# Kernel optimization log

Measured on AMD Instinct MI355X. Metric: run time of the kernel, lower is better.

The kernel has to match this reference:

```python
import jax, jax.numpy as jnp
import numpy as np

B, C, H, W = 4, 128, 64, 64


def setup_inputs() -> dict:
    key = jax.random.key(0)
    ks = jax.random.split(key, 7)
    s = 1.0 / np.sqrt(C)
    return {
        "x": jax.random.normal(ks[0], (B, C, H, W), dtype=jnp.float32),
        "Wq": jax.random.normal(ks[1], (C, C), dtype=jnp.float32) * s,
        "bq": jnp.zeros((C,), dtype=jnp.float32),
        "Wk": jax.random.normal(ks[2], (C, C), dtype=jnp.float32) * s,
        "bk": jnp.zeros((C,), dtype=jnp.float32),
        "Wv": jax.random.normal(ks[3], (C, C), dtype=jnp.float32) * s,
        "bv": jnp.zeros((C,), dtype=jnp.float32),
    }


def reference(x, Wq, bq, Wk, bk, Wv, bv):
    b, c, h, w = x.shape
    n = h * w
    scale = c ** (-0.5)
    # tokens: [B, N, C]
    xt = x.reshape(b, c, n).transpose(0, 2, 1)
    # 1x1 convs == per-token channel GEMMs (out[c'] = sum_c W[c',c] x[c] + b[c'])
    q = jnp.einsum("bnc,dc->bnd", xt, Wq) + bq  # [B, N, C]
    k = jnp.einsum("bnc,dc->bnd", xt, Wk) + bk  # [B, N, C]
    v = jnp.einsum("bnc,dc->bnd", xt, Wv) + bv  # [B, N, C]
    scores = jnp.einsum("bic,bjc->bij", q, k) * scale  # [B, N, N]
    attn = jax.nn.softmax(scores, axis=-1)
    out = jnp.einsum("bij,bjc->bic", attn, v)  # [B, N, C]
    return out.transpose(0, 2, 1).reshape(b, c, h, w)
```

## Files before the change

kernel.cpp:

```cpp
#include <hip/hip_runtime.h>
#include <hip/hip_bf16.h>


#define BATCH 4
#define CH    128
#define NTOK  4096
#define TK    64
#define SCALE 0.08838834764831845f
#define LOG2E 1.4426950408889634f
#define MFIX  16.0f

typedef __attribute__((ext_vector_type(8)))  short short8;
typedef __attribute__((ext_vector_type(4)))  float f32x4;
typedef __attribute__((ext_vector_type(16))) float f32x16;

static __device__ __forceinline__ unsigned short f2bf(float f) {
    __hip_bfloat16 h = (__hip_bfloat16)f;
    return *(const unsigned short*)&h;
}

static __device__ __forceinline__ unsigned cvt_pk_bf16(float lo, float hi) {
    unsigned r;
    asm("v_cvt_pk_bf16_f32 %0, %1, %2" : "=v"(r) : "v"(lo), "v"(hi));
    return r;
}

static __device__ __forceinline__ short8 pack_bf16x8(float4 a, float4 b) {
    union { unsigned u[4]; short8 s8; } f;
    f.u[0] = cvt_pk_bf16(a.x, a.y);
    f.u[1] = cvt_pk_bf16(a.z, a.w);
    f.u[2] = cvt_pk_bf16(b.x, b.y);
    f.u[3] = cvt_pk_bf16(b.z, b.w);
    return f.s8;
}

__global__ __launch_bounds__(256) void proj_mfma_kernel(
    const float* __restrict__ x,
    const float* __restrict__ Wq, const float* __restrict__ Wk,
    const float* __restrict__ Wv,
    const float* __restrict__ bq, const float* __restrict__ bk,
    const float* __restrict__ bv,
    unsigned short* __restrict__ q_ws, unsigned short* __restrict__ k_ws,
    unsigned short* __restrict__ vt_ws)
{
    __shared__ __align__(16) unsigned short Wl[CH * CH];
    __shared__ __align__(16) unsigned short XsT[64 * CH];

    const int t    = threadIdx.x;
    const int w    = t >> 6;
    const int lane = t & 63;
    const int quad = lane >> 4;
    const int c16  = lane & 15;
    const int n0   = blockIdx.x * 64;
    const int b    = blockIdx.y;
    const int z    = blockIdx.z;
    const float* xb = x + (size_t)b * CH * NTOK;
    const float* wm = (z == 0) ? Wq : (z == 1) ? Wk : Wv;

    #pragma unroll
    for (int i = 0; i < 8; ++i) {
        const int f   = i * 256 + t;
        const int row = f >> 4;
        const int u   = f & 15;
        const float* src = wm + f * 8;
        const float4 a = *(const float4*)src;
        const float4 c = *(const float4*)(src + 4);
        *(short8*)&Wl[row * CH + (u ^ (row & 15)) * 8] = pack_bf16x8(a, c);
    }

    {
        const int tok = lane;
        #pragma unroll
        for (int cc = 0; cc < 4; ++cc) {
            const int cb = 32 * w + 8 * cc;
            float xv[8];
            #pragma unroll
            for (int j = 0; j < 8; ++j)
                xv[j] = xb[(size_t)(cb + j) * NTOK + n0 + tok];
            union { unsigned u[4]; short8 s8; } pk;
            #pragma unroll
            for (int j = 0; j < 4; ++j)
                pk.u[j] = cvt_pk_bf16(xv[2 * j], xv[2 * j + 1]);
            const int phys = ((cb >> 3) ^ (tok & 15));
            *(short8*)&XsT[tok * CH + phys * 8] = pk.s8;
        }
    }
    __syncthreads();

    if (z < 2) {
        const float* bias = (z == 0) ? bq : bk;
        unsigned short* dst = (z == 0) ? q_ws : k_ws;
        const float mul = (z == 0) ? (SCALE * LOG2E) : 1.0f;

        short8 xa[4];
        #pragma unroll
        for (int ks = 0; ks < 4; ++ks)
            xa[ks] = *(const short8*)&XsT[(16 * w + c16) * CH + (((4 * ks + quad) ^ c16) << 3)];

        #pragma unroll
        for (int nt = 0; nt < 8; ++nt) {
            f32x4 a = (f32x4){0.f, 0.f, 0.f, 0.f};
            #pragma unroll
            for (int ks = 0; ks < 4; ++ks) {
                const short8 bf = *(const short8*)
                    &Wl[(16 * nt + c16) * CH + (((4 * ks + quad) ^ c16) << 3)];
                a = __builtin_amdgcn_mfma_f32_16x16x32_bf16(xa[ks], bf, a, 0, 0, 0);
            }
            const float bvv = bias[16 * nt + c16];
            #pragma unroll
            for (int r = 0; r < 4; ++r) {
                const int n = n0 + 16 * w + quad * 4 + r;
                dst[((size_t)b * NTOK + n) * CH + 16 * nt + c16] =
                    f2bf((a[r] + bvv) * mul);
            }
        }
    } else {
        #pragma unroll
        for (int nt = 0; nt < 4; ++nt) {
            short8 xbf[4];
            #pragma unroll
            for (int ks = 0; ks < 4; ++ks)
                xbf[ks] = *(const short8*)&XsT[(16 * nt + c16) * CH + (((4 * ks + quad) ^ c16) << 3)];
            #pragma unroll
            for (int mt = 0; mt < 2; ++mt) {
                const int crow16 = 16 * (2 * w + mt);
                f32x4 acc = (f32x4){0.f, 0.f, 0.f, 0.f};
                #pragma unroll
                for (int ks = 0; ks < 4; ++ks) {
                    const short8 wva = *(const short8*)
                        &Wl[(crow16 + c16) * CH + (((4 * ks + quad) ^ c16) << 3)];
                    acc = __builtin_amdgcn_mfma_f32_16x16x32_bf16(wva, xbf[ks], acc, 0, 0, 0);
                }
                #pragma unroll
                for (int r = 0; r < 4; ++r) {
                    const int crow = crow16 + quad * 4 + r;
                    vt_ws[((size_t)b * CH + crow) * NTOK + n0 + 16 * nt + c16] =
                        f2bf(acc[r] + bv[crow]);
                }
            }
        }
    }
}

template <int SPLIT>
__global__ __launch_bounds__(256, 2) void flash_attn_mfma(
    const unsigned short* __restrict__ q_ws,
    const unsigned short* __restrict__ k_ws,
    const unsigned short* __restrict__ vt_ws,
    float* __restrict__ out,
    float* __restrict__ Op, float* __restrict__ l_p)
{
    __shared__ __align__(16) unsigned short KsU[2][TK * CH];
    __shared__ __align__(16) unsigned short VtU[2][CH * TK];

    const int t    = threadIdx.x;
    const int w    = t >> 6;
    const int lane = t & 63;
    const int half = lane >> 5;
    const int l32  = lane & 31;
    const int jc   = blockIdx.y;
    const int b    = blockIdx.z;
    const int n0   = blockIdx.x * 128;
    const int jbeg = jc * (NTOK / SPLIT);
    constexpr int NT = (NTOK / SPLIT) / TK;

    const unsigned short* kg = k_ws  + (size_t)b * NTOK * CH;
    const unsigned short* vg = vt_ws + (size_t)b * CH * NTOK;

    short8 qa[8];
    {
        const unsigned short* qrow =
            q_ws + ((size_t)b * NTOK + n0 + 32 * w + l32) * CH;
        #pragma unroll
        for (int ks = 0; ks < 8; ++ks)
            qa[ks] = *(const short8*)(qrow + ks * 16 + half * 8);
    }

    f32x16 Oa[4];
    #pragma unroll
    for (int ct = 0; ct < 4; ++ct) Oa[ct] = (f32x16)(0.0f);
    float lsum = 0.f;

    const int krl = lane >> 4, ku = lane & 15;
    const int vcl = lane >> 3, vu = lane & 7;

    auto STAGE = [&](int buf, int jj) {
        #pragma unroll
        for (int ci = 0; ci < 4; ++ci) {
            const int row = 16 * w + 4 * ci + krl;
            const int g   = ku ^ (row & 15);
            const unsigned short* src = kg + (size_t)(jj + row) * CH + g * 8;
            __builtin_amdgcn_global_load_lds(
                (const __attribute__((address_space(1))) void*)src,
                (__attribute__((address_space(3))) void*)&KsU[buf][(16 * w + 4 * ci) * CH],
                16, 0, 0);
        }
        #pragma unroll
        for (int ci = 0; ci < 4; ++ci) {
            const int c = 32 * w + 8 * ci + vcl;
            const int g = vu ^ (c & 7);
            const unsigned short* src = vg + (size_t)c * NTOK + jj + g * 8;
            __builtin_amdgcn_global_load_lds(
                (const __attribute__((address_space(1))) void*)src,
                (__attribute__((address_space(3))) void*)&VtU[buf][(32 * w + 8 * ci) * TK],
                16, 0, 0);
        }
    };

    STAGE(0, jbeg);

    int j0 = jbeg;
    for (int tt = 0; tt < NT; ++tt, j0 += TK) {
        const int cur = tt & 1;
        if (tt + 1 < NT) {
            STAGE(cur ^ 1, j0 + TK);
            asm volatile("s_waitcnt vmcnt(8)" ::: "memory");
        } else {
            asm volatile("s_waitcnt vmcnt(0)" ::: "memory");
        }
        __builtin_amdgcn_sched_barrier(0);
        __builtin_amdgcn_s_barrier();
        __builtin_amdgcn_sched_barrier(0);

        const unsigned short* Kc = &KsU[cur][0];
        const unsigned short* Vc = &VtU[cur][0];

        f32x16 s[2];
        s[0] = (f32x16)(-MFIX);
        s[1] = (f32x16)(-MFIX);
        #pragma unroll
        for (int ks = 0; ks < 8; ++ks) {
            const int ph = (2 * ks + half) ^ (l32 & 15);
            const short8 kf0 = *(const short8*)&Kc[l32 * CH + ph * 8];
            const short8 kf1 = *(const short8*)&Kc[(32 + l32) * CH + ph * 8];
            s[0] = __builtin_amdgcn_mfma_f32_32x32x16_bf16(kf0, qa[ks], s[0], 0, 0, 0);
            s[1] = __builtin_amdgcn_mfma_f32_32x32x16_bf16(kf1, qa[ks], s[1], 0, 0, 0);
        }

        short8 pb[4];
        #pragma unroll
        for (int kt = 0; kt < 2; ++kt) {
            float p[16];
            #pragma unroll
            for (int r = 0; r < 16; ++r) p[r] = exp2f(s[kt][r]);
            float a0 = 0.f, a1 = 0.f, a2 = 0.f, a3 = 0.f;
            #pragma unroll
            for (int r = 0; r < 4; ++r) {
                a0 += p[r]; a1 += p[4 + r]; a2 += p[8 + r]; a3 += p[12 + r];
            }
            lsum += (a0 + a1) + (a2 + a3);
            unsigned wd[8];
            #pragma unroll
            for (int i = 0; i < 8; ++i) wd[i] = cvt_pk_bf16(p[2 * i], p[2 * i + 1]);
            auto r02 = __builtin_amdgcn_permlane32_swap(wd[0], wd[2], false, false);
            auto r13 = __builtin_amdgcn_permlane32_swap(wd[1], wd[3], false, false);
            auto r46 = __builtin_amdgcn_permlane32_swap(wd[4], wd[6], false, false);
            auto r57 = __builtin_amdgcn_permlane32_swap(wd[5], wd[7], false, false);
            union { unsigned u[4]; short8 s8; } f0, f1;
            f0.u[0] = r02[0]; f0.u[1] = r13[0]; f0.u[2] = r02[1]; f0.u[3] = r13[1];
            f1.u[0] = r46[0]; f1.u[1] = r57[0]; f1.u[2] = r46[1]; f1.u[3] = r57[1];
            pb[2 * kt + 0] = f0.s8;
            pb[2 * kt + 1] = f1.s8;
        }

        #pragma unroll
        for (int ks2 = 0; ks2 < 4; ++ks2) {
            #pragma unroll
            for (int ct = 0; ct < 4; ++ct) {
                const int ch = 32 * ct + l32;
                const int ph = (2 * ks2 + half) ^ (ch & 7);
                const short8 vf = *(const short8*)&Vc[ch * TK + ph * 8];
                Oa[ct] = __builtin_amdgcn_mfma_f32_32x32x16_bf16(vf, pb[ks2], Oa[ct], 0, 0, 0);
            }
        }
        __builtin_amdgcn_sched_barrier(0);
        __builtin_amdgcn_s_barrier();
        __builtin_amdgcn_sched_barrier(0);
    }

    const float lt = lsum + __shfl_xor(lsum, 32);
    const int n = n0 + 32 * w + l32;

    if constexpr (SPLIT == 1) {
        const float inv = 1.0f / lt;
        #pragma unroll
        for (int ct = 0; ct < 4; ++ct) {
            #pragma unroll
            for (int r = 0; r < 16; ++r) {
                const int c = 32 * ct + (r & 3) + 8 * (r >> 2) + 4 * half;
                out[((size_t)b * CH + c) * NTOK + n] = Oa[ct][r] * inv;
            }
        }
    } else {
        const size_t chunk = (size_t)(b * SPLIT + jc);
        #pragma unroll
        for (int ct = 0; ct < 4; ++ct) {
            #pragma unroll
            for (int r = 0; r < 16; ++r) {
                const int c = 32 * ct + (r & 3) + 8 * (r >> 2) + 4 * half;
                Op[(chunk * CH + c) * NTOK + n] = Oa[ct][r];
            }
        }
        if (half == 0) l_p[chunk * NTOK + n] = lt;
    }
}

template <int SPLIT>
__global__ __launch_bounds__(256) void combine_kernel(
    const float* __restrict__ Op, const float* __restrict__ l_p,
    float* __restrict__ out)
{
    const int b = blockIdx.y;
    const size_t idx = ((size_t)blockIdx.x * 256 + threadIdx.x) * 4;
    const int c = (int)(idx >> 12);
    const int n = (int)(idx & (NTOK - 1));
    float4 acc = make_float4(0.f, 0.f, 0.f, 0.f);
    float4 den = make_float4(0.f, 0.f, 0.f, 0.f);
    #pragma unroll
    for (int j = 0; j < SPLIT; ++j) {
        const size_t chunk = (size_t)(b * SPLIT + j);
        const float4 o = *(const float4*)&Op[(chunk * CH + c) * NTOK + n];
        const float4 d = *(const float4*)&l_p[chunk * NTOK + n];
        acc.x += o.x; acc.y += o.y; acc.z += o.z; acc.w += o.w;
        den.x += d.x; den.y += d.y; den.z += d.z; den.w += d.w;
    }
    float4 r;
    r.x = acc.x / den.x; r.y = acc.y / den.y;
    r.z = acc.z / den.z; r.w = acc.w / den.w;
    *(float4*)&out[((size_t)b * CH * NTOK) + idx] = r;
}

extern "C" void kernel_launch(void* const* d_in, const int* in_sizes, int n_in,
                              void* d_out, int out_size, void* d_ws, size_t ws_size,
                              hipStream_t stream) {
    const float* x  = (const float*)d_in[0];
    const float* Wq = (const float*)d_in[1];
    const float* bq = (const float*)d_in[2];
    const float* Wk = (const float*)d_in[3];
    const float* bk = (const float*)d_in[4];
    const float* Wv = (const float*)d_in[5];
    const float* bv = (const float*)d_in[6];
    float* out = (float*)d_out;

    const size_t QKV = (size_t)BATCH * NTOK * CH;
    unsigned short* q_ws  = (unsigned short*)d_ws;
    unsigned short* k_ws  = q_ws + QKV;
    unsigned short* vt_ws = k_ws + QKV;
    float* Op = (float*)(vt_ws + QKV);

    const size_t baseBytes = 3 * QKV * 2;
    auto needBytes = [&](size_t S) {
        return baseBytes + S * BATCH * NTOK * (size_t)(CH * 4 + 4);
    };

    dim3 gp(NTOK / 64, BATCH, 3);
    proj_mfma_kernel<<<gp, 256, 0, stream>>>(x, Wq, Wk, Wv, bq, bk, bv,
                                             q_ws, k_ws, vt_ws);

    dim3 gc(CH * NTOK / 1024, BATCH);
    if (ws_size >= needBytes(4)) {
        float* l_p = Op + (size_t)4 * BATCH * NTOK * CH;
        dim3 ga(NTOK / 128, 4, BATCH);
        flash_attn_mfma<4><<<ga, 256, 0, stream>>>(q_ws, k_ws, vt_ws, out, Op, l_p);
        combine_kernel<4><<<gc, 256, 0, stream>>>(Op, l_p, out);
    } else if (ws_size >= needBytes(2)) {
        float* l_p = Op + (size_t)2 * BATCH * NTOK * CH;
        dim3 ga(NTOK / 128, 2, BATCH);
        flash_attn_mfma<2><<<ga, 256, 0, stream>>>(q_ws, k_ws, vt_ws, out, Op, l_p);
        combine_kernel<2><<<gc, 256, 0, stream>>>(Op, l_p, out);
    } else {
        dim3 ga(NTOK / 128, 1, BATCH);
        flash_attn_mfma<1><<<ga, 256, 0, stream>>>(q_ws, k_ws, vt_ws, out,
                                                   nullptr, nullptr);
    }
}
```

Baseline: 126.9 us.

## Fuse projection, split attention and combine into one persistent kernel with grid barriers

Replaces the three-launch sequence (projection, split-K flash attention, combine) with a single persistent 512-block kernel. Two software grid barriers built on atomic counters separate the phases, and the projection and attention phases share LDS through a union. The aim is to remove kernel launch gaps and tail effects between stages. In exchange it adds a memset launch, relies on all 512 blocks being co-resident (two per CU) or the barrier deadlocks, and runs the projection phase unevenly, with some blocks doing two units of work.

```diff
diff --git a/kernel.cpp b/kernel.cpp
--- a/kernel.cpp
+++ b/kernel.cpp
@@ -9,6 +9,7 @@
 #define SCALE 0.08838834764831845f
 #define LOG2E 1.4426950408889634f
 #define MFIX  16.0f
+#define GRID  512
 
 typedef __attribute__((ext_vector_type(8)))  short short8;
 typedef __attribute__((ext_vector_type(4)))  float f32x4;
@@ -32,6 +33,318 @@
     f.u[2] = cvt_pk_bf16(b.x, b.y);
     f.u[3] = cvt_pk_bf16(b.z, b.w);
     return f.s8;
+}
+
+static __device__ __forceinline__ void grid_barrier(unsigned* cnt, unsigned* gen) {
+    __syncthreads();
+    __threadfence();
+    if (threadIdx.x == 0) {
+        unsigned prev = __hip_atomic_fetch_add(cnt, 1u, __ATOMIC_ACQ_REL,
+                                               __HIP_MEMORY_SCOPE_AGENT);
+        if (prev == GRID - 1) {
+            __hip_atomic_store(gen, 1u, __ATOMIC_RELEASE,
+                               __HIP_MEMORY_SCOPE_AGENT);
+        } else {
+            while (__hip_atomic_load(gen, __ATOMIC_ACQUIRE,
+                                     __HIP_MEMORY_SCOPE_AGENT) == 0u) {}
+        }
+    }
+    __syncthreads();
+    __threadfence();
+}
+
+__global__ __launch_bounds__(256, 2) void fused_kernel(
+    const float* __restrict__ x,
+    const float* __restrict__ Wq, const float* __restrict__ Wk,
+    const float* __restrict__ Wv,
+    const float* __restrict__ bq, const float* __restrict__ bk,
+    const float* __restrict__ bv,
+    unsigned short* __restrict__ q_ws, unsigned short* __restrict__ k_ws,
+    unsigned short* __restrict__ vt_ws,
+    float* __restrict__ out, float* __restrict__ Op, float* __restrict__ l_p,
+    unsigned* __restrict__ bar)
+{
+    union SMem {
+        struct { unsigned short Wl[CH * CH]; unsigned short XsT[64 * CH]; } p1;
+        struct { unsigned short K[2][TK * CH]; unsigned short V[2][CH * TK]; } p2;
+    };
+    __shared__ __align__(16) SMem sm;
+
+    const int t   = threadIdx.x;
+    const int bid = blockIdx.x;
+
+    {
+        const int w    = t >> 6;
+        const int lane = t & 63;
+        const int quad = lane >> 4;
+        const int c16  = lane & 15;
+        const int nun  = (bid < 256) ? 2 : 1;
+
+        for (int pu = 0; pu < nun; ++pu) {
+            const int uid = (pu == 0) ? bid : 512 + bid;
+            const int z   = uid >> 8;
+            const int rem = uid & 255;
+            const int b   = rem >> 6;
+            const int n0  = (rem & 63) * 64;
+            const float* xb = x + (size_t)b * CH * NTOK;
+            const float* wm = (z == 0) ? Wq : (z == 1) ? Wk : Wv;
+
+            #pragma unroll
+            for (int i = 0; i < 8; ++i) {
+                const int f   = i * 256 + t;
+                const int row = f >> 4;
+                const int u   = f & 15;
+                const float* src = wm + f * 8;
+                const float4 a = *(const float4*)src;
+                const float4 c = *(const float4*)(src + 4);
+                *(short8*)&sm.p1.Wl[row * CH + ((u ^ (row & 15)) << 3)] =
+                    pack_bf16x8(a, c);
+            }
+            {
+                const int tok = lane;
+                #pragma unroll
+                for (int cc = 0; cc < 4; ++cc) {
+                    const int cb = 32 * w + 8 * cc;
+                    float xv[8];
+                    #pragma unroll
+                    for (int j = 0; j < 8; ++j)
+                        xv[j] = xb[(size_t)(cb + j) * NTOK + n0 + tok];
+                    union { unsigned u[4]; short8 s8; } pk;
+                    #pragma unroll
+                    for (int j = 0; j < 4; ++j)
+                        pk.u[j] = cvt_pk_bf16(xv[2 * j], xv[2 * j + 1]);
+                    const int phys = ((cb >> 3) ^ (tok & 15));
+                    *(short8*)&sm.p1.XsT[tok * CH + phys * 8] = pk.s8;
+                }
+            }
+            __syncthreads();
+
+            if (z < 2) {
+                const float* bias = (z == 0) ? bq : bk;
+                unsigned short* dst = (z == 0) ? q_ws : k_ws;
+                const float mul = (z == 0) ? (SCALE * LOG2E) : 1.0f;
+
+                short8 xa[4];
+                #pragma unroll
+                for (int ks = 0; ks < 4; ++ks)
+                    xa[ks] = *(const short8*)
+                        &sm.p1.XsT[(16 * w + c16) * CH + (((4 * ks + quad) ^ c16) << 3)];
+
+                #pragma unroll
+                for (int nt = 0; nt < 8; ++nt) {
+                    f32x4 a = (f32x4){0.f, 0.f, 0.f, 0.f};
+                    #pragma unroll
+                    for (int ks = 0; ks < 4; ++ks) {
+                        const short8 bf = *(const short8*)
+                            &sm.p1.Wl[(16 * nt + c16) * CH + (((4 * ks + quad) ^ c16) << 3)];
+                        a = __builtin_amdgcn_mfma_f32_16x16x32_bf16(xa[ks], bf, a, 0, 0, 0);
+                    }
+                    const float bvv = bias[16 * nt + c16];
+                    #pragma unroll
+                    for (int r = 0; r < 4; ++r) {
+                        const int n = n0 + 16 * w + quad * 4 + r;
+                        dst[((size_t)b * NTOK + n) * CH + 16 * nt + c16] =
+                            f2bf((a[r] + bvv) * mul);
+                    }
+                }
+            } else {
+                #pragma unroll
+                for (int nt = 0; nt < 4; ++nt) {
+                    short8 xbf[4];
+                    #pragma unroll
+                    for (int ks = 0; ks < 4; ++ks)
+                        xbf[ks] = *(const short8*)
+                            &sm.p1.XsT[(16 * nt + c16) * CH + (((4 * ks + quad) ^ c16) << 3)];
+                    #pragma unroll
+                    for (int mt = 0; mt < 2; ++mt) {
+                        const int crow16 = 16 * (2 * w + mt);
+                        f32x4 acc = (f32x4){0.f, 0.f, 0.f, 0.f};
+                        #pragma unroll
+                        for (int ks = 0; ks < 4; ++ks) {
+                            const short8 wva = *(const short8*)
+                                &sm.p1.Wl[(crow16 + c16) * CH + (((4 * ks + quad) ^ c16) << 3)];
+                            acc = __builtin_amdgcn_mfma_f32_16x16x32_bf16(wva, xbf[ks], acc, 0, 0, 0);
+                        }
+                        #pragma unroll
+                        for (int r = 0; r < 4; ++r) {
+                            const int crow = crow16 + quad * 4 + r;
+                            vt_ws[((size_t)b * CH + crow) * NTOK + n0 + 16 * nt + c16] =
+                                f2bf(acc[r] + bv[crow]);
+                        }
+                    }
+                }
+            }
+            __syncthreads();
+        }
+    }
+
+    grid_barrier(bar + 0, bar + 1);
+
+    {
+        const int w    = t >> 6;
+        const int lane = t & 63;
+        const int half = lane >> 5;
+        const int l32  = lane & 31;
+        const int n0   = (bid & 31) * 128;
+        const int jc   = (bid >> 5) & 3;
+        const int b    = bid >> 7;
+        const int jbeg = jc * (NTOK / 4);
+        constexpr int NT = (NTOK / 4) / TK;
+
+        const unsigned short* kg = k_ws  + (size_t)b * NTOK * CH;
+        const unsigned short* vg = vt_ws + (size_t)b * CH * NTOK;
+
+        short8 qa[8];
+        {
+            const unsigned short* qrow =
+                q_ws + ((size_t)b * NTOK + n0 + 32 * w + l32) * CH;
+            #pragma unroll
+            for (int ks = 0; ks < 8; ++ks)
+                qa[ks] = *(const short8*)(qrow + ks * 16 + half * 8);
+        }
+
+        f32x16 Oa[4];
+        #pragma unroll
+        for (int ct = 0; ct < 4; ++ct) Oa[ct] = (f32x16)(0.0f);
+        float lsum = 0.f;
+
+        const int krl = lane >> 4, ku = lane & 15;
+        const int vcl = lane >> 3, vu = lane & 7;
+
+        auto STAGE = [&](int buf, int jj) {
+            #pragma unroll
+            for (int ci = 0; ci < 4; ++ci) {
+                const int row = 16 * w + 4 * ci + krl;
+                const int g   = ku ^ (row & 15);
+                const unsigned short* src = kg + (size_t)(jj + row) * CH + g * 8;
+                __builtin_amdgcn_global_load_lds(
+                    (const __attribute__((address_space(1))) void*)src,
+                    (__attribute__((address_space(3))) void*)&sm.p2.K[buf][(16 * w + 4 * ci) * CH],
+                    16, 0, 0);
+            }
+            #pragma unroll
+            for (int ci = 0; ci < 4; ++ci) {
+                const int c = 32 * w + 8 * ci + vcl;
+                const int g = vu ^ (c & 7);
+                const unsigned short* src = vg + (size_t)c * NTOK + jj + g * 8;
+                __builtin_amdgcn_global_load_lds(
+                    (const __attribute__((address_space(1))) void*)src,
+                    (__attribute__((address_space(3))) void*)&sm.p2.V[buf][(32 * w + 8 * ci) * TK],
+                    16, 0, 0);
+            }
+        };
+
+        STAGE(0, jbeg);
+
+        int j0 = jbeg;
+        for (int tt = 0; tt < NT; ++tt, j0 += TK) {
+            const int cur = tt & 1;
+            if (tt + 1 < NT) {
+                STAGE(cur ^ 1, j0 + TK);
+                asm volatile("s_waitcnt vmcnt(8)" ::: "memory");
+            } else {
+                asm volatile("s_waitcnt vmcnt(0)" ::: "memory");
+            }
+            __builtin_amdgcn_sched_barrier(0);
+            __builtin_amdgcn_s_barrier();
+            __builtin_amdgcn_sched_barrier(0);
+
+            const unsigned short* Kc = &sm.p2.K[cur][0];
+            const unsigned short* Vc = &sm.p2.V[cur][0];
+
+            f32x16 s[2];
+            s[0] = (f32x16)(-MFIX);
+            s[1] = (f32x16)(-MFIX);
+            #pragma unroll
+            for (int ks = 0; ks < 8; ++ks) {
+                const int ph = (2 * ks + half) ^ (l32 & 15);
+                const short8 kf0 = *(const short8*)&Kc[l32 * CH + ph * 8];
+                const short8 kf1 = *(const short8*)&Kc[(32 + l32) * CH + ph * 8];
+                s[0] = __builtin_amdgcn_mfma_f32_32x32x16_bf16(kf0, qa[ks], s[0], 0, 0, 0);
+                s[1] = __builtin_amdgcn_mfma_f32_32x32x16_bf16(kf1, qa[ks], s[1], 0, 0, 0);
+            }
+
+            short8 pb[4];
+            #pragma unroll
+            for (int kt = 0; kt < 2; ++kt) {
+                float p[16];
+                #pragma unroll
+                for (int r = 0; r < 16; ++r) p[r] = exp2f(s[kt][r]);
+                float a0 = 0.f, a1 = 0.f, a2 = 0.f, a3 = 0.f;
+                #pragma unroll
+                for (int r = 0; r < 4; ++r) {
+                    a0 += p[r]; a1 += p[4 + r]; a2 += p[8 + r]; a3 += p[12 + r];
+                }
+                lsum += (a0 + a1) + (a2 + a3);
+                unsigned wd[8];
+                #pragma unroll
+                for (int i = 0; i < 8; ++i) wd[i] = cvt_pk_bf16(p[2 * i], p[2 * i + 1]);
+                auto r02 = __builtin_amdgcn_permlane32_swap(wd[0], wd[2], false, false);
+                auto r13 = __builtin_amdgcn_permlane32_swap(wd[1], wd[3], false, false);
+                auto r46 = __builtin_amdgcn_permlane32_swap(wd[4], wd[6], false, false);
+                auto r57 = __builtin_amdgcn_permlane32_swap(wd[5], wd[7], false, false);
+                union { unsigned u[4]; short8 s8; } f0, f1;
+                f0.u[0] = r02[0]; f0.u[1] = r13[0]; f0.u[2] = r02[1]; f0.u[3] = r13[1];
+                f1.u[0] = r46[0]; f1.u[1] = r57[0]; f1.u[2] = r46[1]; f1.u[3] = r57[1];
+                pb[2 * kt + 0] = f0.s8;
+                pb[2 * kt + 1] = f1.s8;
+            }
+
+            #pragma unroll
+            for (int ks2 = 0; ks2 < 4; ++ks2) {
+                #pragma unroll
+                for (int ct = 0; ct < 4; ++ct) {
+                    const int ch = 32 * ct + l32;
+                    const int ph = (2 * ks2 + half) ^ (ch & 7);
+                    const short8 vf = *(const short8*)&Vc[ch * TK + ph * 8];
+                    Oa[ct] = __builtin_amdgcn_mfma_f32_32x32x16_bf16(vf, pb[ks2], Oa[ct], 0, 0, 0);
+                }
+            }
+            __builtin_amdgcn_sched_barrier(0);
+            __builtin_amdgcn_s_barrier();
+            __builtin_amdgcn_sched_barrier(0);
+        }
+
+        const float lt = lsum + __shfl_xor(lsum, 32);
+        const int n = n0 + 32 * w + l32;
+        const size_t chunk = (size_t)(b * 4 + jc);
+        #pragma unroll
+        for (int ct = 0; ct < 4; ++ct) {
+            #pragma unroll
+            for (int r = 0; r < 16; ++r) {
+                const int c = 32 * ct + (r & 3) + 8 * (r >> 2) + 4 * half;
+                Op[(chunk * CH + c) * NTOK + n] = Oa[ct][r];
+            }
+        }
+        if (half == 0) l_p[chunk * NTOK + n] = lt;
+    }
+
+    grid_barrier(bar + 2, bar + 3);
+
+    {
+        const size_t nf4 = (size_t)BATCH * CH * NTOK / 4;
+        for (size_t fi = (size_t)bid * 256 + t; fi < nf4; fi += (size_t)GRID * 256) {
+            const size_t g = fi * 4;
+            const int b = (int)(g >> 19);
+            const int rem = (int)(g & ((CH * NTOK) - 1));
+            const int c = rem >> 12;
+            const int n = rem & (NTOK - 1);
+            float4 acc = make_float4(0.f, 0.f, 0.f, 0.f);
+            float4 den = make_float4(0.f, 0.f, 0.f, 0.f);
+            #pragma unroll
+            for (int j = 0; j < 4; ++j) {
+                const size_t chunk = (size_t)(b * 4 + j);
+                const float4 o = *(const float4*)&Op[(chunk * CH + c) * NTOK + n];
+                const float4 d = *(const float4*)&l_p[chunk * NTOK + n];
+                acc.x += o.x; acc.y += o.y; acc.z += o.z; acc.w += o.w;
+                den.x += d.x; den.y += d.y; den.z += d.z; den.w += d.w;
+            }
+            float4 r;
+            r.x = acc.x / den.x; r.y = acc.y / den.y;
+            r.z = acc.z / den.z; r.w = acc.w / den.w;
+            *(float4*)&out[g] = r;
+        }
+    }
 }
 
 __global__ __launch_bounds__(256) void proj_mfma_kernel(
@@ -65,9 +378,8 @@
         const float* src = wm + f * 8;
         const float4 a = *(const float4*)src;
         const float4 c = *(const float4*)(src + 4);
-        *(short8*)&Wl[row * CH + (u ^ (row & 15)) * 8] = pack_bf16x8(a, c);
-    }
-
+        *(short8*)&Wl[row * CH + ((u ^ (row & 15)) << 3)] = pack_bf16x8(a, c);
+    }
     {
         const int tok = lane;
         #pragma unroll
@@ -91,12 +403,10 @@
         const float* bias = (z == 0) ? bq : bk;
         unsigned short* dst = (z == 0) ? q_ws : k_ws;
         const float mul = (z == 0) ? (SCALE * LOG2E) : 1.0f;
-
         short8 xa[4];
         #pragma unroll
         for (int ks = 0; ks < 4; ++ks)
             xa[ks] = *(const short8*)&XsT[(16 * w + c16) * CH + (((4 * ks + quad) ^ c16) << 3)];
-
         #pragma unroll
         for (int nt = 0; nt < 8; ++nt) {
             f32x4 a = (f32x4){0.f, 0.f, 0.f, 0.f};
@@ -142,13 +452,11 @@
     }
 }
 
-template <int SPLIT>
-__global__ __launch_bounds__(256, 2) void flash_attn_mfma(
+__global__ __launch_bounds__(256, 2) void flash_attn_s1(
     const unsigned short* __restrict__ q_ws,
     const unsigned short* __restrict__ k_ws,
     const unsigned short* __restrict__ vt_ws,
-    float* __restrict__ out,
-    float* __restrict__ Op, float* __restrict__ l_p)
+    float* __restrict__ out)
 {
     __shared__ __align__(16) unsigned short KsU[2][TK * CH];
     __shared__ __align__(16) unsigned short VtU[2][CH * TK];
@@ -158,11 +466,9 @@
     const int lane = t & 63;
     const int half = lane >> 5;
     const int l32  = lane & 31;
-    const int jc   = blockIdx.y;
     const int b    = blockIdx.z;
     const int n0   = blockIdx.x * 128;
-    const int jbeg = jc * (NTOK / SPLIT);
-    constexpr int NT = (NTOK / SPLIT) / TK;
+    constexpr int NT = NTOK / TK;
 
     const unsigned short* kg = k_ws  + (size_t)b * NTOK * CH;
     const unsigned short* vg = vt_ws + (size_t)b * CH * NTOK;
@@ -175,7 +481,6 @@
         for (int ks = 0; ks < 8; ++ks)
             qa[ks] = *(const short8*)(qrow + ks * 16 + half * 8);
     }
-
     f32x16 Oa[4];
     #pragma unroll
     for (int ct = 0; ct < 4; ++ct) Oa[ct] = (f32x16)(0.0f);
@@ -207,9 +512,8 @@
         }
     };
 
-    STAGE(0, jbeg);
-
-    int j0 = jbeg;
+    STAGE(0, 0);
+    int j0 = 0;
     for (int tt = 0; tt < NT; ++tt, j0 += TK) {
         const int cur = tt & 1;
         if (tt + 1 < NT) {
@@ -236,7 +540,6 @@
             s[0] = __builtin_amdgcn_mfma_f32_32x32x16_bf16(kf0, qa[ks], s[0], 0, 0, 0);
             s[1] = __builtin_amdgcn_mfma_f32_32x32x16_bf16(kf1, qa[ks], s[1], 0, 0, 0);
         }
-
         short8 pb[4];
         #pragma unroll
         for (int kt = 0; kt < 2; ++kt) {
@@ -262,7 +565,6 @@
             pb[2 * kt + 0] = f0.s8;
             pb[2 * kt + 1] = f1.s8;
         }
-
         #pragma unroll
         for (int ks2 = 0; ks2 < 4; ++ks2) {
             #pragma unroll
@@ -280,54 +582,15 @@
 
     const float lt = lsum + __shfl_xor(lsum, 32);
     const int n = n0 + 32 * w + l32;
-
-    if constexpr (SPLIT == 1) {
-        const float inv = 1.0f / lt;
-        #pragma unroll
-        for (int ct = 0; ct < 4; ++ct) {
-            #pragma unroll
-            for (int r = 0; r < 16; ++r) {
-                const int c = 32 * ct + (r & 3) + 8 * (r >> 2) + 4 * half;
-                out[((size_t)b * CH + c) * NTOK + n] = Oa[ct][r] * inv;
-            }
-        }
-    } else {
-        const size_t chunk = (size_t)(b * SPLIT + jc);
-        #pragma unroll
-        for (int ct = 0; ct < 4; ++ct) {
-            #pragma unroll
-            for (int r = 0; r < 16; ++r) {
-                const int c = 32 * ct + (r & 3) + 8 * (r >> 2) + 4 * half;
-                Op[(chunk * CH + c) * NTOK + n] = Oa[ct][r];
-            }
-        }
-        if (half == 0) l_p[chunk * NTOK + n] = lt;
-    }
-}
-
-template <int SPLIT>
-__global__ __launch_bounds__(256) void combine_kernel(
-    const float* __restrict__ Op, const float* __restrict__ l_p,
-    float* __restrict__ out)
-{
-    const int b = blockIdx.y;
-    const size_t idx = ((size_t)blockIdx.x * 256 + threadIdx.x) * 4;
-    const int c = (int)(idx >> 12);
-    const int n = (int)(idx & (NTOK - 1));
-    float4 acc = make_float4(0.f, 0.f, 0.f, 0.f);
-    float4 den = make_float4(0.f, 0.f, 0.f, 0.f);
+    const float inv = 1.0f / lt;
     #pragma unroll
-    for (int j = 0; j < SPLIT; ++j) {
-        const size_t chunk = (size_t)(b * SPLIT + j);
-        const float4 o = *(const float4*)&Op[(chunk * CH + c) * NTOK + n];
-        const float4 d = *(const float4*)&l_p[chunk * NTOK + n];
-        acc.x += o.x; acc.y += o.y; acc.z += o.z; acc.w += o.w;
-        den.x += d.x; den.y += d.y; den.z += d.z; den.w += d.w;
-    }
-    float4 r;
-    r.x = acc.x / den.x; r.y = acc.y / den.y;
-    r.z = acc.z / den.z; r.w = acc.w / den.w;
-    *(float4*)&out[((size_t)b * CH * NTOK) + idx] = r;
+    for (int ct = 0; ct < 4; ++ct) {
+        #pragma unroll
+        for (int r = 0; r < 16; ++r) {
+            const int c = 32 * ct + (r & 3) + 8 * (r >> 2) + 4 * half;
+            out[((size_t)b * CH + c) * NTOK + n] = Oa[ct][r] * inv;
+        }
+    }
 }
 
 extern "C" void kernel_launch(void* const* d_in, const int* in_sizes, int n_in,
@@ -347,30 +610,24 @@
     unsigned short* k_ws  = q_ws + QKV;
     unsigned short* vt_ws = k_ws + QKV;
     float* Op = (float*)(vt_ws + QKV);
+    float* l_p = Op + (size_t)4 * BATCH * NTOK * CH;
+    unsigned* bar = (unsigned*)(l_p + (size_t)4 * BATCH * NTOK);
 
     const size_t baseBytes = 3 * QKV * 2;
-    auto needBytes = [&](size_t S) {
-        return baseBytes + S * BATCH * NTOK * (size_t)(CH * 4 + 4);
-    };
-
-    dim3 gp(NTOK / 64, BATCH, 3);
-    proj_mfma_kernel<<<gp, 256, 0, stream>>>(x, Wq, Wk, Wv, bq, bk, bv,
-                                             q_ws, k_ws, vt_ws);
-
-    dim3 gc(CH * NTOK / 1024, BATCH);
-    if (ws_size >= needBytes(4)) {
-        float* l_p = Op + (size_t)4 * BATCH * NTOK * CH;
-        dim3 ga(NTOK / 128, 4, BATCH);
-        flash_attn_mfma<4><<<ga, 256, 0, stream>>>(q_ws, k_ws, vt_ws, out, Op, l_p);
-        combine_kernel<4><<<gc, 256, 0, stream>>>(Op, l_p, out);
-    } else if (ws_size >= needBytes(2)) {
-        float* l_p = Op + (size_t)2 * BATCH * NTOK * CH;
-        dim3 ga(NTOK / 128, 2, BATCH);
-        flash_attn_mfma<2><<<ga, 256, 0, stream>>>(q_ws, k_ws, vt_ws, out, Op, l_p);
-        combine_kernel<2><<<gc, 256, 0, stream>>>(Op, l_p, out);
+    const size_t need4 = baseBytes
+                       + (size_t)4 * BATCH * NTOK * (CH * 4 + 4)
+                       + 64;
+
+    if (ws_size >= need4) {
+        hipMemsetAsync(bar, 0, 4 * sizeof(unsigned), stream);
+        fused_kernel<<<GRID, 256, 0, stream>>>(x, Wq, Wk, Wv, bq, bk, bv,
+                                               q_ws, k_ws, vt_ws,
+                                               out, Op, l_p, bar);
     } else {
+        dim3 gp(NTOK / 64, BATCH, 3);
+        proj_mfma_kernel<<<gp, 256, 0, stream>>>(x, Wq, Wk, Wv, bq, bk, bv,
+                                                 q_ws, k_ws, vt_ws);
         dim3 ga(NTOK / 128, 1, BATCH);
-        flash_attn_mfma<1><<<ga, 256, 0, stream>>>(q_ws, k_ws, vt_ws, out,
-                                                   nullptr, nullptr);
-    }
-}
+        flash_attn_s1<<<ga, 256, 0, stream>>>(q_ws, k_ws, vt_ws, out);
+    }
+}
```

Result: slower. 376.2 us (+196.5%).

## Process two query sub-tiles per wave to reuse K/V fragments; split KV eightfold

Applied to the files above, without the earlier changes.

Each wave now handles 64 query rows (two 32-row sub-tiles), so every K and V fragment read from LDS feeds two MFMAs instead of one. This halves LDS traffic and global K/V staging per query. The block now covers 256 queries, and the KV split is raised to 8 when the workspace allows, to keep the grid large. In exchange, register pressure roughly doubles for the accumulators and Q fragments, which risks spills or lower occupancy under launch_bounds(256,2), and the combine pass reads more partials.

```diff
diff --git a/kernel.cpp b/kernel.cpp
--- a/kernel.cpp
+++ b/kernel.cpp
@@ -65,9 +65,8 @@
         const float* src = wm + f * 8;
         const float4 a = *(const float4*)src;
         const float4 c = *(const float4*)(src + 4);
-        *(short8*)&Wl[row * CH + (u ^ (row & 15)) * 8] = pack_bf16x8(a, c);
-    }
-
+        *(short8*)&Wl[row * CH + ((u ^ (row & 15)) << 3)] = pack_bf16x8(a, c);
+    }
     {
         const int tok = lane;
         #pragma unroll
@@ -91,12 +90,10 @@
         const float* bias = (z == 0) ? bq : bk;
         unsigned short* dst = (z == 0) ? q_ws : k_ws;
         const float mul = (z == 0) ? (SCALE * LOG2E) : 1.0f;
-
         short8 xa[4];
         #pragma unroll
         for (int ks = 0; ks < 4; ++ks)
             xa[ks] = *(const short8*)&XsT[(16 * w + c16) * CH + (((4 * ks + quad) ^ c16) << 3)];
-
         #pragma unroll
         for (int nt = 0; nt < 8; ++nt) {
             f32x4 a = (f32x4){0.f, 0.f, 0.f, 0.f};
@@ -160,26 +157,29 @@
     const int l32  = lane & 31;
     const int jc   = blockIdx.y;
     const int b    = blockIdx.z;
-    const int n0   = blockIdx.x * 128;
+    const int n0   = blockIdx.x * 256;
     const int jbeg = jc * (NTOK / SPLIT);
     constexpr int NT = (NTOK / SPLIT) / TK;
 
     const unsigned short* kg = k_ws  + (size_t)b * NTOK * CH;
     const unsigned short* vg = vt_ws + (size_t)b * CH * NTOK;
 
-    short8 qa[8];
-    {
+    short8 qa[2][8];
+    #pragma unroll
+    for (int qs = 0; qs < 2; ++qs) {
         const unsigned short* qrow =
-            q_ws + ((size_t)b * NTOK + n0 + 32 * w + l32) * CH;
+            q_ws + ((size_t)b * NTOK + n0 + 64 * w + 32 * qs + l32) * CH;
         #pragma unroll
         for (int ks = 0; ks < 8; ++ks)
-            qa[ks] = *(const short8*)(qrow + ks * 16 + half * 8);
-    }
-
-    f32x16 Oa[4];
-    #pragma unroll
-    for (int ct = 0; ct < 4; ++ct) Oa[ct] = (f32x16)(0.0f);
-    float lsum = 0.f;
+            qa[qs][ks] = *(const short8*)(qrow + ks * 16 + half * 8);
+    }
+
+    f32x16 Oa[2][4];
+    #pragma unroll
+    for (int qs = 0; qs < 2; ++qs)
+        #pragma unroll
+        for (int ct = 0; ct < 4; ++ct) Oa[qs][ct] = (f32x16)(0.0f);
+    float lsum[2] = {0.f, 0.f};
 
     const int krl = lane >> 4, ku = lane & 15;
     const int vcl = lane >> 3, vu = lane & 7;
@@ -225,42 +225,43 @@
         const unsigned short* Kc = &KsU[cur][0];
         const unsigned short* Vc = &VtU[cur][0];
 
-        f32x16 s[2];
-        s[0] = (f32x16)(-MFIX);
-        s[1] = (f32x16)(-MFIX);
-        #pragma unroll
-        for (int ks = 0; ks < 8; ++ks) {
-            const int ph = (2 * ks + half) ^ (l32 & 15);
-            const short8 kf0 = *(const short8*)&Kc[l32 * CH + ph * 8];
-            const short8 kf1 = *(const short8*)&Kc[(32 + l32) * CH + ph * 8];
-            s[0] = __builtin_amdgcn_mfma_f32_32x32x16_bf16(kf0, qa[ks], s[0], 0, 0, 0);
-            s[1] = __builtin_amdgcn_mfma_f32_32x32x16_bf16(kf1, qa[ks], s[1], 0, 0, 0);
-        }
-
-        short8 pb[4];
+        short8 pb[2][4];
         #pragma unroll
         for (int kt = 0; kt < 2; ++kt) {
-            float p[16];
-            #pragma unroll
-            for (int r = 0; r < 16; ++r) p[r] = exp2f(s[kt][r]);
-            float a0 = 0.f, a1 = 0.f, a2 = 0.f, a3 = 0.f;
-            #pragma unroll
-            for (int r = 0; r < 4; ++r) {
-                a0 += p[r]; a1 += p[4 + r]; a2 += p[8 + r]; a3 += p[12 + r];
-            }
-            lsum += (a0 + a1) + (a2 + a3);
-            unsigned wd[8];
-            #pragma unroll
-            for (int i = 0; i < 8; ++i) wd[i] = cvt_pk_bf16(p[2 * i], p[2 * i + 1]);
-            auto r02 = __builtin_amdgcn_permlane32_swap(wd[0], wd[2], false, false);
-            auto r13 = __builtin_amdgcn_permlane32_swap(wd[1], wd[3], false, false);
-            auto r46 = __builtin_amdgcn_permlane32_swap(wd[4], wd[6], false, false);
-            auto r57 = __builtin_amdgcn_permlane32_swap(wd[5], wd[7], false, false);
-            union { unsigned u[4]; short8 s8; } f0, f1;
-            f0.u[0] = r02[0]; f0.u[1] = r13[0]; f0.u[2] = r02[1]; f0.u[3] = r13[1];
-            f1.u[0] = r46[0]; f1.u[1] = r57[0]; f1.u[2] = r46[1]; f1.u[3] = r57[1];
-            pb[2 * kt + 0] = f0.s8;
-            pb[2 * kt + 1] = f1.s8;
+            f32x16 s[2];
+            s[0] = (f32x16)(-MFIX);
+            s[1] = (f32x16)(-MFIX);
+            #pragma unroll
+            for (int ks = 0; ks < 8; ++ks) {
+                const int ph = (2 * ks + half) ^ (l32 & 15);
+                const short8 kf = *(const short8*)&Kc[(32 * kt + l32) * CH + ph * 8];
+                s[0] = __builtin_amdgcn_mfma_f32_32x32x16_bf16(kf, qa[0][ks], s[0], 0, 0, 0);
+                s[1] = __builtin_amdgcn_mfma_f32_32x32x16_bf16(kf, qa[1][ks], s[1], 0, 0, 0);
+            }
+            #pragma unroll
+            for (int qs = 0; qs < 2; ++qs) {
+                float p[16];
+                #pragma unroll
+                for (int r = 0; r < 16; ++r) p[r] = exp2f(s[qs][r]);
+                float a0 = 0.f, a1 = 0.f, a2 = 0.f, a3 = 0.f;
+                #pragma unroll
+                for (int r = 0; r < 4; ++r) {
+                    a0 += p[r]; a1 += p[4 + r]; a2 += p[8 + r]; a3 += p[12 + r];
+                }
+                lsum[qs] += (a0 + a1) + (a2 + a3);
+                unsigned wd[8];
+                #pragma unroll
+                for (int i = 0; i < 8; ++i) wd[i] = cvt_pk_bf16(p[2 * i], p[2 * i + 1]);
+                auto r02 = __builtin_amdgcn_permlane32_swap(wd[0], wd[2], false, false);
+                auto r13 = __builtin_amdgcn_permlane32_swap(wd[1], wd[3], false, false);
+                auto r46 = __builtin_amdgcn_permlane32_swap(wd[4], wd[6], false, false);
+                auto r57 = __builtin_amdgcn_permlane32_swap(wd[5], wd[7], false, false);
+                union { unsigned u[4]; short8 s8; } f0, f1;
+                f0.u[0] = r02[0]; f0.u[1] = r13[0]; f0.u[2] = r02[1]; f0.u[3] = r13[1];
+                f1.u[0] = r46[0]; f1.u[1] = r57[0]; f1.u[2] = r46[1]; f1.u[3] = r57[1];
+                pb[qs][2 * kt + 0] = f0.s8;
+                pb[qs][2 * kt + 1] = f1.s8;
+            }
         }
 
         #pragma unroll
@@ -270,7 +271,8 @@
                 const int ch = 32 * ct + l32;
                 const int ph = (2 * ks2 + half) ^ (ch & 7);
                 const short8 vf = *(const short8*)&Vc[ch * TK + ph * 8];
-                Oa[ct] = __builtin_amdgcn_mfma_f32_32x32x16_bf16(vf, pb[ks2], Oa[ct], 0, 0, 0);
+                Oa[0][ct] = __builtin_amdgcn_mfma_f32_32x32x16_bf16(vf, pb[0][ks2], Oa[0][ct], 0, 0, 0);
+                Oa[1][ct] = __builtin_amdgcn_mfma_f32_32x32x16_bf16(vf, pb[1][ks2], Oa[1][ct], 0, 0, 0);
             }
         }
         __builtin_amdgcn_sched_barrier(0);
@@ -278,30 +280,40 @@
         __builtin_amdgcn_sched_barrier(0);
     }
 
-    const float lt = lsum + __shfl_xor(lsum, 32);
-    const int n = n0 + 32 * w + l32;
+    float lt[2];
+    #pragma unroll
+    for (int qs = 0; qs < 2; ++qs)
+        lt[qs] = lsum[qs] + __shfl_xor(lsum[qs], 32);
 
     if constexpr (SPLIT == 1) {
-        const float inv = 1.0f / lt;
-        #pragma unroll
-        for (int ct = 0; ct < 4; ++ct) {
-            #pragma unroll
-            for (int r = 0; r < 16; ++r) {
-                const int c = 32 * ct + (r & 3) + 8 * (r >> 2) + 4 * half;
-                out[((size_t)b * CH + c) * NTOK + n] = Oa[ct][r] * inv;
+        #pragma unroll
+        for (int qs = 0; qs < 2; ++qs) {
+            const float inv = 1.0f / lt[qs];
+            const int n = n0 + 64 * w + 32 * qs + l32;
+            #pragma unroll
+            for (int ct = 0; ct < 4; ++ct) {
+                #pragma unroll
+                for (int r = 0; r < 16; ++r) {
+                    const int c = 32 * ct + (r & 3) + 8 * (r >> 2) + 4 * half;
+                    out[((size_t)b * CH + c) * NTOK + n] = Oa[qs][ct][r] * inv;
+                }
             }
         }
     } else {
         const size_t chunk = (size_t)(b * SPLIT + jc);
         #pragma unroll
-        for (int ct = 0; ct < 4; ++ct) {
-            #pragma unroll
-            for (int r = 0; r < 16; ++r) {
-                const int c = 32 * ct + (r & 3) + 8 * (r >> 2) + 4 * half;
-                Op[(chunk * CH + c) * NTOK + n] = Oa[ct][r];
-            }
-        }
-        if (half == 0) l_p[chunk * NTOK + n] = lt;
+        for (int qs = 0; qs < 2; ++qs) {
+            const int n = n0 + 64 * w + 32 * qs + l32;
+            #pragma unroll
+            for (int ct = 0; ct < 4; ++ct) {
+                #pragma unroll
+                for (int r = 0; r < 16; ++r) {
+                    const int c = 32 * ct + (r & 3) + 8 * (r >> 2) + 4 * half;
+                    Op[(chunk * CH + c) * NTOK + n] = Oa[qs][ct][r];
+                }
+            }
+            if (half == 0) l_p[chunk * NTOK + n] = lt[qs];
+        }
     }
 }
 
@@ -358,18 +370,18 @@
                                              q_ws, k_ws, vt_ws);
 
     dim3 gc(CH * NTOK / 1024, BATCH);
-    if (ws_size >= needBytes(4)) {
+    if (ws_size >= needBytes(8)) {
+        float* l_p = Op + (size_t)8 * BATCH * NTOK * CH;
+        dim3 ga(NTOK / 256, 8, BATCH);
+        flash_attn_mfma<8><<<ga, 256, 0, stream>>>(q_ws, k_ws, vt_ws, out, Op, l_p);
+        combine_kernel<8><<<gc, 256, 0, stream>>>(Op, l_p, out);
+    } else if (ws_size >= needBytes(4)) {
         float* l_p = Op + (size_t)4 * BATCH * NTOK * CH;
-        dim3 ga(NTOK / 128, 4, BATCH);
+        dim3 ga(NTOK / 256, 4, BATCH);
         flash_attn_mfma<4><<<ga, 256, 0, stream>>>(q_ws, k_ws, vt_ws, out, Op, l_p);
         combine_kernel<4><<<gc, 256, 0, stream>>>(Op, l_p, out);
-    } else if (ws_size >= needBytes(2)) {
-        float* l_p = Op + (size_t)2 * BATCH * NTOK * CH;
-        dim3 ga(NTOK / 128, 2, BATCH);
-        flash_attn_mfma<2><<<ga, 256, 0, stream>>>(q_ws, k_ws, vt_ws, out, Op, l_p);
-        combine_kernel<2><<<gc, 256, 0, stream>>>(Op, l_p, out);
     } else {
-        dim3 ga(NTOK / 128, 1, BATCH);
+        dim3 ga(NTOK / 256, 1, BATCH);
         flash_attn_mfma<1><<<ga, 256, 0, stream>>>(q_ws, k_ws, vt_ws, out,
                                                    nullptr, nullptr);
     }
```

Measured after the change: 215.7 us. 70.0% more time.

## Store K in MFMA fragment order and load it directly into registers

Applied to the files above, without the earlier changes.

The projection kernel now writes K in a pre-swizzled fragment layout that matches the 32x32x16 MFMA operand order. The attention kernel drops the K shared-memory staging buffer and each wave loads its K fragments straight from global memory into registers, prefetching the next tile after the QK MFMAs. This removes LDS traffic and half the shared-memory footprint, which may allow more occupancy. In exchange, each of the four waves re-reads the same K tile from global/L2 and the prefetch adds 64 extra VGPRs under a 2-blocks-per-CU launch bound.

```diff
diff --git a/kernel.cpp b/kernel.cpp
--- a/kernel.cpp
+++ b/kernel.cpp
@@ -40,7 +40,7 @@
     const float* __restrict__ Wv,
     const float* __restrict__ bq, const float* __restrict__ bk,
     const float* __restrict__ bv,
-    unsigned short* __restrict__ q_ws, unsigned short* __restrict__ k_ws,
+    unsigned short* __restrict__ q_ws, unsigned short* __restrict__ kf_ws,
     unsigned short* __restrict__ vt_ws)
 {
     __shared__ __align__(16) unsigned short Wl[CH * CH];
@@ -65,9 +65,8 @@
         const float* src = wm + f * 8;
         const float4 a = *(const float4*)src;
         const float4 c = *(const float4*)(src + 4);
-        *(short8*)&Wl[row * CH + (u ^ (row & 15)) * 8] = pack_bf16x8(a, c);
-    }
-
+        *(short8*)&Wl[row * CH + ((u ^ (row & 15)) << 3)] = pack_bf16x8(a, c);
+    }
     {
         const int tok = lane;
         #pragma unroll
@@ -89,14 +88,11 @@
 
     if (z < 2) {
         const float* bias = (z == 0) ? bq : bk;
-        unsigned short* dst = (z == 0) ? q_ws : k_ws;
         const float mul = (z == 0) ? (SCALE * LOG2E) : 1.0f;
-
         short8 xa[4];
         #pragma unroll
         for (int ks = 0; ks < 4; ++ks)
             xa[ks] = *(const short8*)&XsT[(16 * w + c16) * CH + (((4 * ks + quad) ^ c16) << 3)];
-
         #pragma unroll
         for (int nt = 0; nt < 8; ++nt) {
             f32x4 a = (f32x4){0.f, 0.f, 0.f, 0.f};
@@ -110,8 +106,15 @@
             #pragma unroll
             for (int r = 0; r < 4; ++r) {
                 const int n = n0 + 16 * w + quad * 4 + r;
-                dst[((size_t)b * NTOK + n) * CH + 16 * nt + c16] =
-                    f2bf((a[r] + bvv) * mul);
+                if (z == 0) {
+                    q_ws[((size_t)b * NTOK + n) * CH + 16 * nt + c16] =
+                        f2bf((a[r] + bvv) * mul);
+                } else {
+                    const size_t idx =
+                        (((size_t)b * (NTOK >> 5) + (n >> 5)) * 8 + nt) * 512
+                        + ((n & 31) + 32 * (c16 >> 3)) * 8 + (c16 & 7);
+                    kf_ws[idx] = f2bf(a[r] + bvv);
+                }
             }
         }
     } else {
@@ -145,12 +148,11 @@
 template <int SPLIT>
 __global__ __launch_bounds__(256, 2) void flash_attn_mfma(
     const unsigned short* __restrict__ q_ws,
-    const unsigned short* __restrict__ k_ws,
+    const unsigned short* __restrict__ kf_ws,
     const unsigned short* __restrict__ vt_ws,
     float* __restrict__ out,
     float* __restrict__ Op, float* __restrict__ l_p)
 {
-    __shared__ __align__(16) unsigned short KsU[2][TK * CH];
     __shared__ __align__(16) unsigned short VtU[2][CH * TK];
 
     const int t    = threadIdx.x;
@@ -163,8 +165,9 @@
     const int n0   = blockIdx.x * 128;
     const int jbeg = jc * (NTOK / SPLIT);
     constexpr int NT = (NTOK / SPLIT) / TK;
-
-    const unsigned short* kg = k_ws  + (size_t)b * NTOK * CH;
+    static_assert(NT >= 2, "need at least 2 tiles");
+
+    const unsigned short* kg = kf_ws + (size_t)b * NTOK * CH;
     const unsigned short* vg = vt_ws + (size_t)b * CH * NTOK;
 
     short8 qa[8];
@@ -181,20 +184,9 @@
     for (int ct = 0; ct < 4; ++ct) Oa[ct] = (f32x16)(0.0f);
     float lsum = 0.f;
 
-    const int krl = lane >> 4, ku = lane & 15;
     const int vcl = lane >> 3, vu = lane & 7;
 
-    auto STAGE = [&](int buf, int jj) {
-        #pragma unroll
-        for (int ci = 0; ci < 4; ++ci) {
-            const int row = 16 * w + 4 * ci + krl;
-            const int g   = ku ^ (row & 15);
-            const unsigned short* src = kg + (size_t)(jj + row) * CH + g * 8;
-            __builtin_amdgcn_global_load_lds(
-                (const __attribute__((address_space(1))) void*)src,
-                (__attribute__((address_space(3))) void*)&KsU[buf][(16 * w + 4 * ci) * CH],
-                16, 0, 0);
-        }
+    auto V_DMA = [&](int buf, int jj) {
         #pragma unroll
         for (int ci = 0; ci < 4; ++ci) {
             const int c = 32 * w + 8 * ci + vcl;
@@ -207,13 +199,24 @@
         }
     };
 
-    STAGE(0, jbeg);
+    short8 kf[2][8];
+    auto KF_LOAD = [&](int jj) {
+        const unsigned short* kb = kg + (size_t)(jj >> 5) * 8 * 512;
+        #pragma unroll
+        for (int kt = 0; kt < 2; ++kt)
+            #pragma unroll
+            for (int ks = 0; ks < 8; ++ks)
+                kf[kt][ks] = *(const short8*)(kb + ((kt * 8 + ks) * 64 + lane) * 8);
+    };
+
+    V_DMA(0, jbeg);
+    KF_LOAD(jbeg);
 
     int j0 = jbeg;
     for (int tt = 0; tt < NT; ++tt, j0 += TK) {
         const int cur = tt & 1;
         if (tt + 1 < NT) {
-            STAGE(cur ^ 1, j0 + TK);
+            V_DMA(cur ^ 1, j0 + TK);
             asm volatile("s_waitcnt vmcnt(8)" ::: "memory");
         } else {
             asm volatile("s_waitcnt vmcnt(0)" ::: "memory");
@@ -222,20 +225,17 @@
         __builtin_amdgcn_s_barrier();
         __builtin_amdgcn_sched_barrier(0);
 
-        const unsigned short* Kc = &KsU[cur][0];
-        const unsigned short* Vc = &VtU[cur][0];
-
         f32x16 s[2];
         s[0] = (f32x16)(-MFIX);
         s[1] = (f32x16)(-MFIX);
         #pragma unroll
         for (int ks = 0; ks < 8; ++ks) {
-            const int ph = (2 * ks + half) ^ (l32 & 15);
-            const short8 kf0 = *(const short8*)&Kc[l32 * CH + ph * 8];
-            const short8 kf1 = *(const short8*)&Kc[(32 + l32) * CH + ph * 8];
-            s[0] = __builtin_amdgcn_mfma_f32_32x32x16_bf16(kf0, qa[ks], s[0], 0, 0, 0);
-            s[1] = __builtin_amdgcn_mfma_f32_32x32x16_bf16(kf1, qa[ks], s[1], 0, 0, 0);
-        }
+            s[0] = __builtin_amdgcn_mfma_f32_32x32x16_bf16(kf[0][ks], qa[ks], s[0], 0, 0, 0);
+            s[1] = __builtin_amdgcn_mfma_f32_32x32x16_bf16(kf[1][ks], qa[ks], s[1], 0, 0, 0);
+        }
+        __builtin_amdgcn_sched_barrier(0);
+        if (tt + 1 < NT) KF_LOAD(j0 + TK);
+        __builtin_amdgcn_sched_barrier(0);
 
         short8 pb[4];
         #pragma unroll
@@ -269,7 +269,7 @@
             for (int ct = 0; ct < 4; ++ct) {
                 const int ch = 32 * ct + l32;
                 const int ph = (2 * ks2 + half) ^ (ch & 7);
-                const short8 vf = *(const short8*)&Vc[ch * TK + ph * 8];
+                const short8 vf = *(const short8*)&VtU[cur][ch * TK + ph * 8];
                 Oa[ct] = __builtin_amdgcn_mfma_f32_32x32x16_bf16(vf, pb[ks2], Oa[ct], 0, 0, 0);
             }
         }
@@ -344,8 +344,8 @@
 
     const size_t QKV = (size_t)BATCH * NTOK * CH;
     unsigned short* q_ws  = (unsigned short*)d_ws;
-    unsigned short* k_ws  = q_ws + QKV;
-    unsigned short* vt_ws = k_ws + QKV;
+    unsigned short* kf_ws = q_ws + QKV;
+    unsigned short* vt_ws = kf_ws + QKV;
     float* Op = (float*)(vt_ws + QKV);
 
     const size_t baseBytes = 3 * QKV * 2;
@@ -355,22 +355,22 @@
 
     dim3 gp(NTOK / 64, BATCH, 3);
     proj_mfma_kernel<<<gp, 256, 0, stream>>>(x, Wq, Wk, Wv, bq, bk, bv,
-                                             q_ws, k_ws, vt_ws);
+                                             q_ws, kf_ws, vt_ws);
 
     dim3 gc(CH * NTOK / 1024, BATCH);
     if (ws_size >= needBytes(4)) {
         float* l_p = Op + (size_t)4 * BATCH * NTOK * CH;
         dim3 ga(NTOK / 128, 4, BATCH);
-        flash_attn_mfma<4><<<ga, 256, 0, stream>>>(q_ws, k_ws, vt_ws, out, Op, l_p);
+        flash_attn_mfma<4><<<ga, 256, 0, stream>>>(q_ws, kf_ws, vt_ws, out, Op, l_p);
         combine_kernel<4><<<gc, 256, 0, stream>>>(Op, l_p, out);
     } else if (ws_size >= needBytes(2)) {
         float* l_p = Op + (size_t)2 * BATCH * NTOK * CH;
         dim3 ga(NTOK / 128, 2, BATCH);
-        flash_attn_mfma<2><<<ga, 256, 0, stream>>>(q_ws, k_ws, vt_ws, out, Op, l_p);
+        flash_attn_mfma<2><<<ga, 256, 0, stream>>>(q_ws, kf_ws, vt_ws, out, Op, l_p);
         combine_kernel<2><<<gc, 256, 0, stream>>>(Op, l_p, out);
     } else {
         dim3 ga(NTOK / 128, 1, BATCH);
-        flash_attn_mfma<1><<<ga, 256, 0, stream>>>(q_ws, k_ws, vt_ws, out,
+        flash_attn_mfma<1><<<ga, 256, 0, stream>>>(q_ws, kf_ws, vt_ws, out,
                                                    nullptr, nullptr);
     }
 }
```

After: 128.6 us. Within noise of the previous version (+1.4%).
